# Kernel tuning notes

Measured on AMD Instinct MI355X. Metric: run time of the kernel, lower is better.

## Reference

```python
import jax, jax.numpy as jnp
import numpy as np

N = 50000      # nodes
E = 800000     # edges (avg degree 16)
IN_DIM = 128
HIDDEN = 128
HEADS = 4
OUT = HIDDEN // HEADS  # 32 per-head out dim
NEG_SLOPE = 0.2        # DGL GATConv default leaky_relu slope


def setup_inputs() -> dict:
    key = jax.random.key(0)
    ks = jax.random.split(key, 12)
    x = jax.random.normal(ks[0], (N, IN_DIM), dtype=jnp.float32)
    src = jax.random.randint(ks[1], (E,), 0, N)
    dst = jax.random.randint(ks[2], (E,), 0, N)
    s = 0.1
    # layer 1 params
    W1 = jax.random.normal(ks[3], (IN_DIM, HEADS * OUT), dtype=jnp.float32) * s
    al1 = jax.random.normal(ks[4], (HEADS, OUT), dtype=jnp.float32) * s
    ar1 = jax.random.normal(ks[5], (HEADS, OUT), dtype=jnp.float32) * s
    b1 = jnp.zeros((HEADS * OUT,), dtype=jnp.float32)
    # layer 2 params (input = flattened heads of layer 1 = HIDDEN)
    W2 = jax.random.normal(ks[6], (HIDDEN, HEADS * OUT), dtype=jnp.float32) * s
    al2 = jax.random.normal(ks[7], (HEADS, OUT), dtype=jnp.float32) * s
    ar2 = jax.random.normal(ks[8], (HEADS, OUT), dtype=jnp.float32) * s
    b2 = jnp.zeros((HEADS * OUT,), dtype=jnp.float32)
    return {"x": x, "W1": W1, "al1": al1, "ar1": ar1, "b1": b1,
            "W2": W2, "al2": al2, "ar2": ar2, "b2": b2,
            "src": src, "dst": dst}


def gat_layer(x, W, a_l, a_r, b, src, dst):
    # x: [N, in], W: [in, H*D], a_l/a_r: [H, D], b: [H*D]
    z = (x @ W).reshape(N, HEADS, OUT)                # [N,H,D]
    el = jnp.sum(z * a_l[None], axis=-1)              # [N,H]
    er = jnp.sum(z * a_r[None], axis=-1)              # [N,H]
    e = jax.nn.leaky_relu(el[src] + er[dst], NEG_SLOPE)  # [E,H]
    # segment softmax over incoming edges of each dst node
    m = jax.ops.segment_max(e, dst, num_segments=N)   # [N,H]
    ex = jnp.exp(e - m[dst])                          # [E,H]
    s = jax.ops.segment_sum(ex, dst, num_segments=N)  # [N,H]
    alpha = ex / s[dst]                               # [E,H]
    out = jax.ops.segment_sum(z[src] * alpha[:, :, None], dst, num_segments=N)
    return out + b.reshape(1, HEADS, OUT)             # [N,H,D]


def reference(x, W1, al1, ar1, b1, W2, al2, ar2, b2, src, dst):
    # dropout is eval-mode (identity)
    h = gat_layer(x, W1, al1, ar1, b1, src, dst)      # [N,H,D]
    h = jax.nn.relu(h).reshape(N, HIDDEN)             # flatten heads between layers
    out = gat_layer(h, W2, al2, ar2, b2, src, dst)    # [N,H,D]
    return out
```

## Files before the change

kernel.cpp:

```cpp
#include <hip/hip_runtime.h>
#include <hip/hip_bf16.h>
#include <math.h>

#define N_NODES 50000
#define N_EDGES 800000
#define DIM 128
#define HEADS 4
#define CAP 64
#define NEG_SLOPE 0.2f
#define GEMM_BLKS 782
#define NBUCK 782
#define CAPB 1280
#define P1_BLKS 200
#define P1_EPB 4000

typedef __attribute__((ext_vector_type(8))) short bf16x8;
typedef __attribute__((ext_vector_type(4))) float f32x4;

__device__ __forceinline__ short f2bf_rne(float x) {
    __hip_bfloat16 h = __float2bfloat16(x);
    return *(short*)&h;
}
__device__ __forceinline__ float lrelu(float v) {
    return v > 0.f ? v : NEG_SLOPE * v;
}

__global__ __launch_bounds__(256) void prep_kernel(
    const float* __restrict__ W1, const float* __restrict__ W2,
    short* __restrict__ Wth, short* __restrict__ Wtl, int* __restrict__ gcur) {
    int t = blockIdx.x * blockDim.x + threadIdx.x;
    if (t < 2 * DIM * DIM) {
        int lay = t >> 14;
        int k = (t >> 7) & 127;
        int n = t & 127;
        float w = (lay ? W2 : W1)[k * DIM + n];
        int bits = __float_as_int(w);
        short hi = (short)(bits >> 16);
        float hif = __int_as_float(bits & 0xFFFF0000);
        Wth[lay * DIM * DIM + n * DIM + k] = hi;
        Wtl[lay * DIM * DIM + n * DIM + k] = f2bf_rne(w - hif);
    }
    if (t < NBUCK) gcur[t] = 0;
}

template <int AF32>
__device__ __forceinline__ void gemm_eler_body(
    int blk, int tid,
    const void* __restrict__ Xv, const short* __restrict__ Wth,
    const short* __restrict__ Wtl, const float* __restrict__ al,
    const float* __restrict__ ar, short* __restrict__ Zb,
    float* __restrict__ el, float* __restrict__ er, int nrows) {
    int wv = tid >> 6, lane = tid & 63;
    int row0 = blk * 64 + wv * 16;
    int c = lane & 15;
    int g = lane >> 4;
    int rA = row0 + c;
    int rAc = rA < nrows ? rA : nrows - 1;
    int koff = g * 8;

    f32x4 acc[8];
#pragma unroll
    for (int n = 0; n < 8; ++n) acc[n] = (f32x4){0.f, 0.f, 0.f, 0.f};

#pragma unroll
    for (int ks = 0; ks < 4; ++ks) {
        int k0 = ks * 32 + koff;
        bf16x8 ah, alo;
        if (AF32) {
            const float* X = (const float*)Xv;
            float4 xa = *(const float4*)&X[(size_t)rAc * DIM + k0];
            float4 xb = *(const float4*)&X[(size_t)rAc * DIM + k0 + 4];
            float xs[8] = {xa.x, xa.y, xa.z, xa.w, xb.x, xb.y, xb.z, xb.w};
#pragma unroll
            for (int j = 0; j < 8; ++j) {
                int bits = __float_as_int(xs[j]);
                ah[j] = (short)(bits >> 16);
                float hif = __int_as_float(bits & 0xFFFF0000);
                alo[j] = f2bf_rne(xs[j] - hif);
            }
        } else {
            const short* Xb = (const short*)Xv;
            ah = *(const bf16x8*)&Xb[(size_t)rAc * DIM + k0];
        }
#pragma unroll
        for (int n = 0; n < 8; ++n) {
            int ncol = n * 16 + c;
            bf16x8 bh = *(const bf16x8*)&Wth[ncol * DIM + k0];
            bf16x8 bl = *(const bf16x8*)&Wtl[ncol * DIM + k0];
            acc[n] = __builtin_amdgcn_mfma_f32_16x16x32_bf16(ah, bh, acc[n], 0, 0, 0);
            if (AF32)
                acc[n] = __builtin_amdgcn_mfma_f32_16x16x32_bf16(alo, bh, acc[n], 0, 0, 0);
            acc[n] = __builtin_amdgcn_mfma_f32_16x16x32_bf16(ah, bl, acc[n], 0, 0, 0);
        }
    }

    int rb = row0 + g * 4;
#pragma unroll
    for (int n = 0; n < 8; ++n) {
#pragma unroll
        for (int r = 0; r < 4; ++r) {
            int row = rb + r;
            if (row < nrows)
                Zb[(size_t)row * DIM + n * 16 + c] = f2bf_rne(acc[n][r]);
        }
    }

    f32x4 elv[4], erv[4];
#pragma unroll
    for (int r = 0; r < 4; ++r) { elv[r] = (f32x4){0,0,0,0}; erv[r] = (f32x4){0,0,0,0}; }
#pragma unroll
    for (int n = 0; n < 8; ++n) {
        int h = n >> 1;
        int idx = ((n & 1) << 4) + c;
        float av = al[h * 32 + idx];
        float bv = ar[h * 32 + idx];
#pragma unroll
        for (int r = 0; r < 4; ++r) {
            elv[r][h] += acc[n][r] * av;
            erv[r][h] += acc[n][r] * bv;
        }
    }
#pragma unroll
    for (int m = 1; m <= 8; m <<= 1) {
#pragma unroll
        for (int r = 0; r < 4; ++r) {
#pragma unroll
            for (int h = 0; h < 4; ++h) {
                elv[r][h] += __shfl_xor(elv[r][h], m);
                erv[r][h] += __shfl_xor(erv[r][h], m);
            }
        }
    }
    if (c < 4) {
        int row = rb + c;
        if (row < nrows) {
            f32x4 eo = c == 0 ? elv[0] : c == 1 ? elv[1] : c == 2 ? elv[2] : elv[3];
            f32x4 ro = c == 0 ? erv[0] : c == 1 ? erv[1] : c == 2 ? erv[2] : erv[3];
            *(float4*)&el[row * 4] = make_float4(eo[0], eo[1], eo[2], eo[3]);
            *(float4*)&er[row * 4] = make_float4(ro[0], ro[1], ro[2], ro[3]);
        }
    }
}

__global__ __launch_bounds__(256) void fused_gemm_pass1_kernel(
    const float* __restrict__ X, const short* __restrict__ Wth,
    const short* __restrict__ Wtl, const float* __restrict__ al,
    const float* __restrict__ ar, short* __restrict__ Zb,
    float* __restrict__ el, float* __restrict__ er,
    const int* __restrict__ src, const int* __restrict__ dst,
    int* __restrict__ gcur, int2* __restrict__ pairs) {
    if (blockIdx.x < GEMM_BLKS) {
        gemm_eler_body<1>(blockIdx.x, threadIdx.x, X, Wth, Wtl, al, ar, Zb, el, er, N_NODES);
        return;
    }
    __shared__ int hist[NBUCK], base_s[NBUCK], cur[NBUCK];
    int tid = threadIdx.x;
    for (int b = tid; b < NBUCK; b += 256) { hist[b] = 0; cur[b] = 0; }
    __syncthreads();
    int blk = blockIdx.x - GEMM_BLKS;
    int e0 = blk * P1_EPB;
    int e1 = e0 + P1_EPB; if (e1 > N_EDGES) e1 = N_EDGES;
    for (int i = e0 + tid; i < e1; i += 256)
        atomicAdd(&hist[dst[i] >> 6], 1);
    __syncthreads();
    for (int b = tid; b < NBUCK; b += 256)
        if (hist[b]) base_s[b] = atomicAdd(&gcur[b], hist[b]);
    __syncthreads();
    for (int i = e0 + tid; i < e1; i += 256) {
        int d = dst[i];
        int b = d >> 6;
        int pos = base_s[b] + atomicAdd(&cur[b], 1);
        if (pos < CAPB) pairs[b * CAPB + pos] = make_int2(src[i], d);
    }
}

__global__ __launch_bounds__(256) void gemm_eler_bf16_kernel(
    const short* __restrict__ X, const short* __restrict__ Wth,
    const short* __restrict__ Wtl, const float* __restrict__ al,
    const float* __restrict__ ar, short* __restrict__ Zb,
    float* __restrict__ el, float* __restrict__ er) {
    gemm_eler_body<0>(blockIdx.x, threadIdx.x, X, Wth, Wtl, al, ar, Zb, el, er, N_NODES);
}

__global__ __launch_bounds__(256) void gat_kernel(
    const int* __restrict__ gcur, const int2* __restrict__ pairs,
    const short* __restrict__ Zb, const float* __restrict__ el,
    const float* __restrict__ er, const float* __restrict__ bias,
    void* __restrict__ out, int mode) {
    __shared__ int fine[16][68];
    __shared__ int lcnt[16];
    __shared__ float stage[4][4][64];
    int tid = threadIdx.x;
    int bkt = blockIdx.x >> 2;
    int q = blockIdx.x & 3;
    int nbase = (bkt << 6) + (q << 4);
    if (tid < 16) lcnt[tid] = 0;
    __syncthreads();
    int ne = gcur[bkt]; if (ne > CAPB) ne = CAPB;
    const int2* pb = pairs + (size_t)bkt * CAPB;
    for (int i = tid; i < ne; i += 256) {
        int2 p = pb[i];
        int ln = p.y & 63;
        if ((ln >> 4) == q) {
            int pos = atomicAdd(&lcnt[ln & 15], 1);
            if (pos < CAP) fine[ln & 15][pos] = p.x;
        }
    }
    __syncthreads();

    int wv = tid >> 6, lane = tid & 63, h = lane >> 4;
    const char* zbase = (const char*)Zb + lane * 4;
    float2 bb = *(const float2*)&bias[lane * 2];
#pragma unroll
    for (int u = 0; u < 4; ++u) {
        int n = (wv << 2) + u;
        int node = nbase + n;
        int d = lcnt[n]; d = d > CAP ? CAP : d;

        float p0 = 0.f, p1 = 0.f, p2 = 0.f, p3 = 0.f;
        if (lane < d) {
            int s = fine[n][lane];
            float4 er4 = *(const float4*)&er[node * HEADS];
            float4 e4 = *(const float4*)&el[s * HEADS];
            p0 = __expf(lrelu(e4.x + er4.x));
            p1 = __expf(lrelu(e4.y + er4.y));
            p2 = __expf(lrelu(e4.z + er4.z));
            p3 = __expf(lrelu(e4.w + er4.w));
        }
        stage[wv][0][lane] = p0;
        stage[wv][1][lane] = p1;
        stage[wv][2][lane] = p2;
        stage[wv][3][lane] = p3;

        float ax = 0.f, ay = 0.f, sm = 0.f;
        int j = 0;
        for (; j + 4 <= d; j += 4) {
            int4 s4 = *(const int4*)&fine[n][j];
            float4 p4 = *(const float4*)&stage[wv][h][j];
            int zz0 = *(const int*)(zbase + ((size_t)s4.x << 8));
            int zz1 = *(const int*)(zbase + ((size_t)s4.y << 8));
            int zz2 = *(const int*)(zbase + ((size_t)s4.z << 8));
            int zz3 = *(const int*)(zbase + ((size_t)s4.w << 8));
            ax += p4.x * __int_as_float(zz0 << 16);
            ay += p4.x * __int_as_float(zz0 & 0xFFFF0000);
            ax += p4.y * __int_as_float(zz1 << 16);
            ay += p4.y * __int_as_float(zz1 & 0xFFFF0000);
            ax += p4.z * __int_as_float(zz2 << 16);
            ay += p4.z * __int_as_float(zz2 & 0xFFFF0000);
            ax += p4.w * __int_as_float(zz3 << 16);
            ay += p4.w * __int_as_float(zz3 & 0xFFFF0000);
            sm += (p4.x + p4.y) + (p4.z + p4.w);
        }
        for (; j < d; ++j) {
            int s = fine[n][j];
            float pv = stage[wv][h][j];
            int zz = *(const int*)(zbase + ((size_t)s << 8));
            ax += pv * __int_as_float(zz << 16);
            ay += pv * __int_as_float(zz & 0xFFFF0000);
            sm += pv;
        }

        if (node < N_NODES) {
            float inv = sm > 0.f ? 1.f / sm : 0.f;
            float ox = ax * inv + bb.x;
            float oy = ay * inv + bb.y;
            if (mode) {
                ox = fmaxf(ox, 0.f); oy = fmaxf(oy, 0.f);
                unsigned int pk = (unsigned int)(unsigned short)f2bf_rne(ox) |
                                  ((unsigned int)(unsigned short)f2bf_rne(oy) << 16);
                ((unsigned int*)out)[(size_t)node * 64 + lane] = pk;
            } else {
                *(float2*)((float*)out + (size_t)node * DIM + lane * 2) =
                    make_float2(ox, oy);
            }
        }
    }
}

extern "C" void kernel_launch(void* const* d_in, const int* in_sizes, int n_in,
                              void* d_out, int out_size, void* d_ws, size_t ws_size,
                              hipStream_t stream) {
    const float* x   = (const float*)d_in[0];
    const float* W1  = (const float*)d_in[1];
    const float* al1 = (const float*)d_in[2];
    const float* ar1 = (const float*)d_in[3];
    const float* b1  = (const float*)d_in[4];
    const float* W2  = (const float*)d_in[5];
    const float* al2 = (const float*)d_in[6];
    const float* ar2 = (const float*)d_in[7];
    const float* b2  = (const float*)d_in[8];
    const int* src   = (const int*)d_in[9];
    const int* dst   = (const int*)d_in[10];

    char* ws = (char*)d_ws;
    short* h1   = (short*)ws; ws += (size_t)N_NODES * DIM * sizeof(short);
    short* Zb   = (short*)ws; ws += (size_t)N_NODES * DIM * sizeof(short);
    float* el   = (float*)ws; ws += (size_t)N_NODES * HEADS * sizeof(float);
    float* er   = (float*)ws; ws += (size_t)N_NODES * HEADS * sizeof(float);
    int2*  pairs = (int2*)ws; ws += (size_t)NBUCK * CAPB * sizeof(int2);
    short* Wth  = (short*)ws; ws += (size_t)2 * DIM * DIM * sizeof(short);
    short* Wtl  = (short*)ws; ws += (size_t)2 * DIM * DIM * sizeof(short);
    int*   gcur = (int*)ws;   ws += (size_t)NBUCK * sizeof(int);

    const int BLK = 256;
    int grid_gat = NBUCK * 4;

    prep_kernel<<<128, BLK, 0, stream>>>(W1, W2, Wth, Wtl, gcur);
    fused_gemm_pass1_kernel<<<GEMM_BLKS + P1_BLKS, BLK, 0, stream>>>(
        x, Wth, Wtl, al1, ar1, Zb, el, er, src, dst, gcur, pairs);
    gat_kernel<<<grid_gat, BLK, 0, stream>>>(gcur, pairs, Zb, el, er, b1, h1, 1);
    gemm_eler_bf16_kernel<<<GEMM_BLKS, BLK, 0, stream>>>(h1, Wth + DIM * DIM,
                                                         Wtl + DIM * DIM,
                                                         al2, ar2, Zb, el, er);
    gat_kernel<<<grid_gat, BLK, 0, stream>>>(gcur, pairs, Zb, el, er, b2, d_out, 0);
}
```

Baseline: 169.5 us.

## Fuse layer-1 aggregation with layer-2 GEMM and attention logits in one kernel

Layer-1 GAT aggregation now keeps its 16 ReLU'd output rows in shared memory and immediately runs the layer-2 bf16 MFMA GEMM plus el/er reduction on them. This drops the separate GEMM kernel launch and the h1 round trip through global memory. The gather loop is unrolled to 8 edges for more memory-level parallelism, and the edge-bucketing pass uses twice as many blocks with half the edges each. Layer-2 buffers are separated so the fused kernel does not overwrite layer-1 data still being read. The cost is extra shared memory and a block-wide sync in the aggregation kernel, which may lower occupancy.

```diff
diff --git a/kernel.cpp b/kernel.cpp
--- a/kernel.cpp
+++ b/kernel.cpp
@@ -11,8 +11,8 @@
 #define GEMM_BLKS 782
 #define NBUCK 782
 #define CAPB 1280
-#define P1_BLKS 200
-#define P1_EPB 4000
+#define P1_BLKS 400
+#define P1_EPB 2000
 
 typedef __attribute__((ext_vector_type(8))) short bf16x8;
 typedef __attribute__((ext_vector_type(4))) float f32x4;
@@ -24,6 +24,8 @@
 __device__ __forceinline__ float lrelu(float v) {
     return v > 0.f ? v : NEG_SLOPE * v;
 }
+__device__ __forceinline__ float blo(int z) { return __int_as_float(z << 16); }
+__device__ __forceinline__ float bhi(int z) { return __int_as_float(z & 0xFFFF0000); }
 
 __global__ __launch_bounds__(256) void prep_kernel(
     const float* __restrict__ W1, const float* __restrict__ W2,
@@ -43,10 +45,9 @@
     if (t < NBUCK) gcur[t] = 0;
 }
 
-template <int AF32>
 __device__ __forceinline__ void gemm_eler_body(
     int blk, int tid,
-    const void* __restrict__ Xv, const short* __restrict__ Wth,
+    const float* __restrict__ X, const short* __restrict__ Wth,
     const short* __restrict__ Wtl, const float* __restrict__ al,
     const float* __restrict__ ar, short* __restrict__ Zb,
     float* __restrict__ el, float* __restrict__ er, int nrows) {
@@ -65,22 +66,16 @@
 #pragma unroll
     for (int ks = 0; ks < 4; ++ks) {
         int k0 = ks * 32 + koff;
+        float4 xa = *(const float4*)&X[(size_t)rAc * DIM + k0];
+        float4 xb = *(const float4*)&X[(size_t)rAc * DIM + k0 + 4];
+        float xs[8] = {xa.x, xa.y, xa.z, xa.w, xb.x, xb.y, xb.z, xb.w};
         bf16x8 ah, alo;
-        if (AF32) {
-            const float* X = (const float*)Xv;
-            float4 xa = *(const float4*)&X[(size_t)rAc * DIM + k0];
-            float4 xb = *(const float4*)&X[(size_t)rAc * DIM + k0 + 4];
-            float xs[8] = {xa.x, xa.y, xa.z, xa.w, xb.x, xb.y, xb.z, xb.w};
-#pragma unroll
-            for (int j = 0; j < 8; ++j) {
-                int bits = __float_as_int(xs[j]);
-                ah[j] = (short)(bits >> 16);
-                float hif = __int_as_float(bits & 0xFFFF0000);
-                alo[j] = f2bf_rne(xs[j] - hif);
-            }
-        } else {
-            const short* Xb = (const short*)Xv;
-            ah = *(const bf16x8*)&Xb[(size_t)rAc * DIM + k0];
+#pragma unroll
+        for (int j = 0; j < 8; ++j) {
+            int bits = __float_as_int(xs[j]);
+            ah[j] = (short)(bits >> 16);
+            float hif = __int_as_float(bits & 0xFFFF0000);
+            alo[j] = f2bf_rne(xs[j] - hif);
         }
 #pragma unroll
         for (int n = 0; n < 8; ++n) {
@@ -88,8 +83,7 @@
             bf16x8 bh = *(const bf16x8*)&Wth[ncol * DIM + k0];
             bf16x8 bl = *(const bf16x8*)&Wtl[ncol * DIM + k0];
             acc[n] = __builtin_amdgcn_mfma_f32_16x16x32_bf16(ah, bh, acc[n], 0, 0, 0);
-            if (AF32)
-                acc[n] = __builtin_amdgcn_mfma_f32_16x16x32_bf16(alo, bh, acc[n], 0, 0, 0);
+            acc[n] = __builtin_amdgcn_mfma_f32_16x16x32_bf16(alo, bh, acc[n], 0, 0, 0);
             acc[n] = __builtin_amdgcn_mfma_f32_16x16x32_bf16(ah, bl, acc[n], 0, 0, 0);
         }
     }
@@ -150,7 +144,7 @@
     const int* __restrict__ src, const int* __restrict__ dst,
     int* __restrict__ gcur, int2* __restrict__ pairs) {
     if (blockIdx.x < GEMM_BLKS) {
-        gemm_eler_body<1>(blockIdx.x, threadIdx.x, X, Wth, Wtl, al, ar, Zb, el, er, N_NODES);
+        gemm_eler_body(blockIdx.x, threadIdx.x, X, Wth, Wtl, al, ar, Zb, el, er, N_NODES);
         return;
     }
     __shared__ int hist[NBUCK], base_s[NBUCK], cur[NBUCK];
@@ -174,19 +168,181 @@
     }
 }
 
-__global__ __launch_bounds__(256) void gemm_eler_bf16_kernel(
-    const short* __restrict__ X, const short* __restrict__ Wth,
-    const short* __restrict__ Wtl, const float* __restrict__ al,
-    const float* __restrict__ ar, short* __restrict__ Zb,
-    float* __restrict__ el, float* __restrict__ er) {
-    gemm_eler_body<0>(blockIdx.x, threadIdx.x, X, Wth, Wtl, al, ar, Zb, el, er, N_NODES);
-}
-
-__global__ __launch_bounds__(256) void gat_kernel(
+#define GATHER_LOOP(FROW, STG, D, AX, AY, SM)                                   \
+    {                                                                           \
+        int j = 0;                                                              \
+        for (; j + 8 <= (D); j += 8) {                                          \
+            int4 sA = *(const int4*)&FROW[j];                                   \
+            int4 sB = *(const int4*)&FROW[j + 4];                               \
+            float4 pA = *(const float4*)&STG[j];                                \
+            float4 pB = *(const float4*)&STG[j + 4];                            \
+            int z0 = *(const int*)(zbase + ((size_t)sA.x << 8));                \
+            int z1 = *(const int*)(zbase + ((size_t)sA.y << 8));                \
+            int z2 = *(const int*)(zbase + ((size_t)sA.z << 8));                \
+            int z3 = *(const int*)(zbase + ((size_t)sA.w << 8));                \
+            int z4 = *(const int*)(zbase + ((size_t)sB.x << 8));                \
+            int z5 = *(const int*)(zbase + ((size_t)sB.y << 8));                \
+            int z6 = *(const int*)(zbase + ((size_t)sB.z << 8));                \
+            int z7 = *(const int*)(zbase + ((size_t)sB.w << 8));                \
+            AX += pA.x * blo(z0); AY += pA.x * bhi(z0);                         \
+            AX += pA.y * blo(z1); AY += pA.y * bhi(z1);                         \
+            AX += pA.z * blo(z2); AY += pA.z * bhi(z2);                         \
+            AX += pA.w * blo(z3); AY += pA.w * bhi(z3);                         \
+            AX += pB.x * blo(z4); AY += pB.x * bhi(z4);                         \
+            AX += pB.y * blo(z5); AY += pB.y * bhi(z5);                         \
+            AX += pB.z * blo(z6); AY += pB.z * bhi(z6);                         \
+            AX += pB.w * blo(z7); AY += pB.w * bhi(z7);                         \
+            SM += (pA.x + pA.y) + (pA.z + pA.w) + (pB.x + pB.y) + (pB.z + pB.w);\
+        }                                                                       \
+        for (; j + 4 <= (D); j += 4) {                                          \
+            int4 sA = *(const int4*)&FROW[j];                                   \
+            float4 pA = *(const float4*)&STG[j];                                \
+            int z0 = *(const int*)(zbase + ((size_t)sA.x << 8));                \
+            int z1 = *(const int*)(zbase + ((size_t)sA.y << 8));                \
+            int z2 = *(const int*)(zbase + ((size_t)sA.z << 8));                \
+            int z3 = *(const int*)(zbase + ((size_t)sA.w << 8));                \
+            AX += pA.x * blo(z0); AY += pA.x * bhi(z0);                         \
+            AX += pA.y * blo(z1); AY += pA.y * bhi(z1);                         \
+            AX += pA.z * blo(z2); AY += pA.z * bhi(z2);                         \
+            AX += pA.w * blo(z3); AY += pA.w * bhi(z3);                         \
+            SM += (pA.x + pA.y) + (pA.z + pA.w);                                \
+        }                                                                       \
+        for (; j < (D); ++j) {                                                  \
+            int s = FROW[j];                                                    \
+            float pv = STG[j];                                                  \
+            int zz = *(const int*)(zbase + ((size_t)s << 8));                   \
+            AX += pv * blo(zz); AY += pv * bhi(zz);                             \
+            SM += pv;                                                           \
+        }                                                                       \
+    }
+
+__global__ __launch_bounds__(256) void gat1_gemm2_kernel(
     const int* __restrict__ gcur, const int2* __restrict__ pairs,
-    const short* __restrict__ Zb, const float* __restrict__ el,
-    const float* __restrict__ er, const float* __restrict__ bias,
-    void* __restrict__ out, int mode) {
+    const short* __restrict__ Zb1, const float* __restrict__ el1,
+    const float* __restrict__ er1, const float* __restrict__ b1,
+    const short* __restrict__ Wth2, const short* __restrict__ Wtl2,
+    const float* __restrict__ al2, const float* __restrict__ ar2,
+    short* __restrict__ Zb2, float* __restrict__ el2, float* __restrict__ er2) {
+    __shared__ int fine[16][68];
+    __shared__ int lcnt[16];
+    __shared__ float stage[4][4][64];
+    __shared__ unsigned int hh[16][68];
+    int tid = threadIdx.x;
+    int bkt = blockIdx.x >> 2;
+    int q = blockIdx.x & 3;
+    int nbase = (bkt << 6) + (q << 4);
+    if (tid < 16) lcnt[tid] = 0;
+    __syncthreads();
+    int ne = gcur[bkt]; if (ne > CAPB) ne = CAPB;
+    const int2* pb = pairs + (size_t)bkt * CAPB;
+    for (int i = tid; i < ne; i += 256) {
+        int2 p = pb[i];
+        int ln = p.y & 63;
+        if ((ln >> 4) == q) {
+            int pos = atomicAdd(&lcnt[ln & 15], 1);
+            if (pos < CAP) fine[ln & 15][pos] = p.x;
+        }
+    }
+    __syncthreads();
+
+    int wv = tid >> 6, lane = tid & 63, h = lane >> 4;
+    const char* zbase = (const char*)Zb1 + lane * 4;
+    float2 bb = *(const float2*)&b1[lane * 2];
+#pragma unroll
+    for (int u = 0; u < 4; ++u) {
+        int n = (wv << 2) + u;
+        int node = nbase + n;
+        int d = lcnt[n]; d = d > CAP ? CAP : d;
+
+        float p0 = 0.f, p1 = 0.f, p2 = 0.f, p3 = 0.f;
+        if (lane < d) {
+            int s = fine[n][lane];
+            float4 er4 = *(const float4*)&er1[node * HEADS];
+            float4 e4 = *(const float4*)&el1[s * HEADS];
+            p0 = __expf(lrelu(e4.x + er4.x));
+            p1 = __expf(lrelu(e4.y + er4.y));
+            p2 = __expf(lrelu(e4.z + er4.z));
+            p3 = __expf(lrelu(e4.w + er4.w));
+        }
+        stage[wv][0][lane] = p0;
+        stage[wv][1][lane] = p1;
+        stage[wv][2][lane] = p2;
+        stage[wv][3][lane] = p3;
+
+        float ax = 0.f, ay = 0.f, sm = 0.f;
+        const int* frow = &fine[n][0];
+        const float* stg = &stage[wv][h][0];
+        GATHER_LOOP(frow, stg, d, ax, ay, sm)
+
+        float inv = sm > 0.f ? 1.f / sm : 0.f;
+        float ox = fmaxf(ax * inv + bb.x, 0.f);
+        float oy = fmaxf(ay * inv + bb.y, 0.f);
+        hh[n][lane] = (unsigned int)(unsigned short)f2bf_rne(ox) |
+                      ((unsigned int)(unsigned short)f2bf_rne(oy) << 16);
+    }
+    __syncthreads();
+
+    int c = lane & 15, g = lane >> 4;
+    f32x4 acc[2];
+    acc[0] = (f32x4){0.f, 0.f, 0.f, 0.f};
+    acc[1] = (f32x4){0.f, 0.f, 0.f, 0.f};
+#pragma unroll
+    for (int ks = 0; ks < 4; ++ks) {
+        int k0 = ks * 32 + g * 8;
+        bf16x8 ah = *(const bf16x8*)((const short*)&hh[c][0] + k0);
+#pragma unroll
+        for (int n2 = 0; n2 < 2; ++n2) {
+            int ncol = wv * 32 + n2 * 16 + c;
+            bf16x8 bh = *(const bf16x8*)&Wth2[ncol * DIM + k0];
+            bf16x8 bl = *(const bf16x8*)&Wtl2[ncol * DIM + k0];
+            acc[n2] = __builtin_amdgcn_mfma_f32_16x16x32_bf16(ah, bh, acc[n2], 0, 0, 0);
+            acc[n2] = __builtin_amdgcn_mfma_f32_16x16x32_bf16(ah, bl, acc[n2], 0, 0, 0);
+        }
+    }
+    int rb = nbase + g * 4;
+#pragma unroll
+    for (int n2 = 0; n2 < 2; ++n2) {
+#pragma unroll
+        for (int r = 0; r < 4; ++r) {
+            int row = rb + r;
+            if (row < N_NODES)
+                Zb2[(size_t)row * DIM + wv * 32 + n2 * 16 + c] = f2bf_rne(acc[n2][r]);
+        }
+    }
+    float elv0 = 0.f, elv1 = 0.f, elv2 = 0.f, elv3 = 0.f;
+    float erv0 = 0.f, erv1 = 0.f, erv2 = 0.f, erv3 = 0.f;
+#pragma unroll
+    for (int n2 = 0; n2 < 2; ++n2) {
+        float av = al2[wv * 32 + n2 * 16 + c];
+        float bv = ar2[wv * 32 + n2 * 16 + c];
+        elv0 += acc[n2][0] * av; erv0 += acc[n2][0] * bv;
+        elv1 += acc[n2][1] * av; erv1 += acc[n2][1] * bv;
+        elv2 += acc[n2][2] * av; erv2 += acc[n2][2] * bv;
+        elv3 += acc[n2][3] * av; erv3 += acc[n2][3] * bv;
+    }
+#pragma unroll
+    for (int m = 1; m <= 8; m <<= 1) {
+        elv0 += __shfl_xor(elv0, m); erv0 += __shfl_xor(erv0, m);
+        elv1 += __shfl_xor(elv1, m); erv1 += __shfl_xor(erv1, m);
+        elv2 += __shfl_xor(elv2, m); erv2 += __shfl_xor(erv2, m);
+        elv3 += __shfl_xor(elv3, m); erv3 += __shfl_xor(erv3, m);
+    }
+    if (c < 4) {
+        int row = rb + c;
+        if (row < N_NODES) {
+            float eo = c == 0 ? elv0 : c == 1 ? elv1 : c == 2 ? elv2 : elv3;
+            float ro = c == 0 ? erv0 : c == 1 ? erv1 : c == 2 ? erv2 : erv3;
+            el2[row * HEADS + wv] = eo;
+            er2[row * HEADS + wv] = ro;
+        }
+    }
+}
+
+__global__ __launch_bounds__(256) void gat2_kernel(
+    const int* __restrict__ gcur, const int2* __restrict__ pairs,
+    const short* __restrict__ Zb2, const float* __restrict__ el2,
+    const float* __restrict__ er2, const float* __restrict__ b2,
+    float* __restrict__ out) {
     __shared__ int fine[16][68];
     __shared__ int lcnt[16];
     __shared__ float stage[4][4][64];
@@ -209,8 +365,8 @@
     __syncthreads();
 
     int wv = tid >> 6, lane = tid & 63, h = lane >> 4;
-    const char* zbase = (const char*)Zb + lane * 4;
-    float2 bb = *(const float2*)&bias[lane * 2];
+    const char* zbase = (const char*)Zb2 + lane * 4;
+    float2 bb = *(const float2*)&b2[lane * 2];
 #pragma unroll
     for (int u = 0; u < 4; ++u) {
         int n = (wv << 2) + u;
@@ -220,8 +376,8 @@
         float p0 = 0.f, p1 = 0.f, p2 = 0.f, p3 = 0.f;
         if (lane < d) {
             int s = fine[n][lane];
-            float4 er4 = *(const float4*)&er[node * HEADS];
-            float4 e4 = *(const float4*)&el[s * HEADS];
+            float4 er4 = *(const float4*)&er2[node * HEADS];
+            float4 e4 = *(const float4*)&el2[s * HEADS];
             p0 = __expf(lrelu(e4.x + er4.x));
             p1 = __expf(lrelu(e4.y + er4.y));
             p2 = __expf(lrelu(e4.z + er4.z));
@@ -233,46 +389,15 @@
         stage[wv][3][lane] = p3;
 
         float ax = 0.f, ay = 0.f, sm = 0.f;
-        int j = 0;
-        for (; j + 4 <= d; j += 4) {
-            int4 s4 = *(const int4*)&fine[n][j];
-            float4 p4 = *(const float4*)&stage[wv][h][j];
-            int zz0 = *(const int*)(zbase + ((size_t)s4.x << 8));
-            int zz1 = *(const int*)(zbase + ((size_t)s4.y << 8));
-            int zz2 = *(const int*)(zbase + ((size_t)s4.z << 8));
-            int zz3 = *(const int*)(zbase + ((size_t)s4.w << 8));
-            ax += p4.x * __int_as_float(zz0 << 16);
-            ay += p4.x * __int_as_float(zz0 & 0xFFFF0000);
-            ax += p4.y * __int_as_float(zz1 << 16);
-            ay += p4.y * __int_as_float(zz1 & 0xFFFF0000);
-            ax += p4.z * __int_as_float(zz2 << 16);
-            ay += p4.z * __int_as_float(zz2 & 0xFFFF0000);
-            ax += p4.w * __int_as_float(zz3 << 16);
-            ay += p4.w * __int_as_float(zz3 & 0xFFFF0000);
-            sm += (p4.x + p4.y) + (p4.z + p4.w);
-        }
-        for (; j < d; ++j) {
-            int s = fine[n][j];
-            float pv = stage[wv][h][j];
-            int zz = *(const int*)(zbase + ((size_t)s << 8));
-            ax += pv * __int_as_float(zz << 16);
-            ay += pv * __int_as_float(zz & 0xFFFF0000);
-            sm += pv;
-        }
+        const int* frow = &fine[n][0];
+        const float* stg = &stage[wv][h][0];
+        GATHER_LOOP(frow, stg, d, ax, ay, sm)
 
         if (node < N_NODES) {
             float inv = sm > 0.f ? 1.f / sm : 0.f;
             float ox = ax * inv + bb.x;
             float oy = ay * inv + bb.y;
-            if (mode) {
-                ox = fmaxf(ox, 0.f); oy = fmaxf(oy, 0.f);
-                unsigned int pk = (unsigned int)(unsigned short)f2bf_rne(ox) |
-                                  ((unsigned int)(unsigned short)f2bf_rne(oy) << 16);
-                ((unsigned int*)out)[(size_t)node * 64 + lane] = pk;
-            } else {
-                *(float2*)((float*)out + (size_t)node * DIM + lane * 2) =
-                    make_float2(ox, oy);
-            }
+            *(float2*)&out[(size_t)node * DIM + lane * 2] = make_float2(ox, oy);
         }
     }
 }
@@ -293,10 +418,12 @@
     const int* dst   = (const int*)d_in[10];
 
     char* ws = (char*)d_ws;
-    short* h1   = (short*)ws; ws += (size_t)N_NODES * DIM * sizeof(short);
-    short* Zb   = (short*)ws; ws += (size_t)N_NODES * DIM * sizeof(short);
-    float* el   = (float*)ws; ws += (size_t)N_NODES * HEADS * sizeof(float);
-    float* er   = (float*)ws; ws += (size_t)N_NODES * HEADS * sizeof(float);
+    short* Zb1  = (short*)ws; ws += (size_t)N_NODES * DIM * sizeof(short);
+    short* Zb2  = (short*)ws; ws += (size_t)N_NODES * DIM * sizeof(short);
+    float* el1  = (float*)ws; ws += (size_t)N_NODES * HEADS * sizeof(float);
+    float* er1  = (float*)ws; ws += (size_t)N_NODES * HEADS * sizeof(float);
+    float* el2  = (float*)ws; ws += (size_t)N_NODES * HEADS * sizeof(float);
+    float* er2  = (float*)ws; ws += (size_t)N_NODES * HEADS * sizeof(float);
     int2*  pairs = (int2*)ws; ws += (size_t)NBUCK * CAPB * sizeof(int2);
     short* Wth  = (short*)ws; ws += (size_t)2 * DIM * DIM * sizeof(short);
     short* Wtl  = (short*)ws; ws += (size_t)2 * DIM * DIM * sizeof(short);
@@ -307,10 +434,10 @@
 
     prep_kernel<<<128, BLK, 0, stream>>>(W1, W2, Wth, Wtl, gcur);
     fused_gemm_pass1_kernel<<<GEMM_BLKS + P1_BLKS, BLK, 0, stream>>>(
-        x, Wth, Wtl, al1, ar1, Zb, el, er, src, dst, gcur, pairs);
-    gat_kernel<<<grid_gat, BLK, 0, stream>>>(gcur, pairs, Zb, el, er, b1, h1, 1);
-    gemm_eler_bf16_kernel<<<GEMM_BLKS, BLK, 0, stream>>>(h1, Wth + DIM * DIM,
-                                                         Wtl + DIM * DIM,
-                                                         al2, ar2, Zb, el, er);
-    gat_kernel<<<grid_gat, BLK, 0, stream>>>(gcur, pairs, Zb, el, er, b2, d_out, 0);
-}
+        x, Wth, Wtl, al1, ar1, Zb1, el1, er1, src, dst, gcur, pairs);
+    gat1_gemm2_kernel<<<grid_gat, BLK, 0, stream>>>(
+        gcur, pairs, Zb1, el1, er1, b1,
+        Wth + DIM * DIM, Wtl + DIM * DIM, al2, ar2, Zb2, el2, er2);
+    gat2_kernel<<<grid_gat, BLK, 0, stream>>>(gcur, pairs, Zb2, el2, er2, b2,
+                                              (float*)d_out);
+}
```

Result: faster. 144.1 us, median of 2 (-15.0%).
